# Optimization experiments

Measured on AMD Instinct MI355X. Metric: run time of the kernel, lower is better.

Reference implementation:

```python
import jax, jax.numpy as jnp
import numpy as np

N, D_IN, D_OUT, E = 8192, 1024, 1024, 8

def setup_inputs() -> dict:
    key = jax.random.key(0)
    ks = jax.random.split(key, 5)
    x = jax.random.normal(ks[0], (N, D_IN), dtype=jnp.float32)
    # expert weights stacked: [E, D_IN, D_OUT], bias [E, D_OUT]
    We = jax.random.normal(ks[1], (E, D_IN, D_OUT), dtype=jnp.float32) / np.sqrt(D_IN)
    be = jax.random.normal(ks[2], (E, D_OUT), dtype=jnp.float32) * 0.01
    # gating net: Linear(D_IN -> E)
    Wg = jax.random.normal(ks[3], (D_IN, E), dtype=jnp.float32) / np.sqrt(D_IN)
    bg = jax.random.normal(ks[4], (E,), dtype=jnp.float32) * 0.01
    return {"x": x, "We": We, "be": be, "Wg": Wg, "bg": bg}

def reference(x, We, be, Wg, bg):
    # gate: softmax over experts  [N, E]
    gate_probs = jax.nn.softmax(x @ Wg + bg, axis=-1)
    # all experts run densely on every token: [N, E, D_OUT]
    expert_out = jnp.einsum('ni,eio->neo', x, We) + be[None, :, :]
    # gate-weighted sum over experts: [N, D_OUT]
    return jnp.einsum('neo,ne->no', expert_out, gate_probs)
```

## Files before the change

kernel.cpp:

```cpp
#include <hip/hip_runtime.h>
#include <hip/hip_bf16.h>

#define N_TOK 8192
#define DIN   1024
#define DOUT  1024
#define NE    8
#define KTOT  (NE * DIN)
#define BM    128
#define BN    128
#define NKC   (KTOT / 32)

typedef __attribute__((ext_vector_type(4))) float f32x4;
typedef __attribute__((ext_vector_type(8))) short short8;
typedef unsigned int u32;

__device__ __forceinline__ ushort f2bf(float f) {
    u32 u = __float_as_uint(f);
    u32 r = (u + 0x7fffu + ((u >> 16) & 1u)) >> 16;
    return (ushort)r;
}

__device__ __forceinline__ void gload_lds16(const void* gp, void* lp) {
    __builtin_amdgcn_global_load_lds(
        (const __attribute__((address_space(1))) u32*)gp,
        (__attribute__((address_space(3))) u32*)lp, 16, 0, 0);
}

#define PH_BAR()  __builtin_amdgcn_s_barrier()
#define VMCNT4()  asm volatile("s_waitcnt vmcnt(4)" ::: "memory")
#define VMCNT0()  asm volatile("s_waitcnt vmcnt(0)" ::: "memory")

__global__ void gate_kernel(const float* __restrict__ x, const float* __restrict__ Wg,
                            const float* __restrict__ bg, float* __restrict__ g) {
    int w = threadIdx.x >> 6, lane = threadIdx.x & 63;
    int n = blockIdx.x * 4 + w;
    const float* xr = x + (size_t)n * DIN;
    float p[NE];
#pragma unroll
    for (int e = 0; e < NE; ++e) p[e] = 0.f;
    for (int i = lane; i < DIN; i += 64) {
        float xv = xr[i];
        const float* wr_ = Wg + i * NE;
#pragma unroll
        for (int e = 0; e < NE; ++e) p[e] = fmaf(xv, wr_[e], p[e]);
    }
#pragma unroll
    for (int off = 32; off > 0; off >>= 1) {
#pragma unroll
        for (int e = 0; e < NE; ++e) p[e] += __shfl_down(p[e], off);
    }
    if (lane == 0) {
        float l2[NE], m = -1e30f;
#pragma unroll
        for (int e = 0; e < NE; ++e) { l2[e] = p[e] + bg[e]; m = fmaxf(m, l2[e]); }
        float s = 0.f;
#pragma unroll
        for (int e = 0; e < NE; ++e) { l2[e] = expf(l2[e] - m); s += l2[e]; }
        float inv = 1.f / s;
#pragma unroll
        for (int e = 0; e < NE; ++e) g[n * NE + e] = l2[e] * inv;
    }
}

__global__ void transpose_w2_kernel(const float* __restrict__ We, ushort* __restrict__ B2) {
    __shared__ float tile[64][65];
    int kb = blockIdx.x * 64, ob = blockIdx.y * 64;
    int t = threadIdx.x;
#pragma unroll
    for (int ph = 0; ph < 16; ++ph) {
        int idx = ph * 256 + t;
        int r = idx >> 6, c = idx & 63;
        tile[r][c] = We[(size_t)(kb + r) * DOUT + ob + c];
    }
    __syncthreads();
#pragma unroll
    for (int ph = 0; ph < 4; ++ph) {
        int widx = ph * 256 + t;
        int o_loc = widx >> 4;
        int k_loc = (widx & 15) * 4;
        int kc = (kb + k_loc) >> 5;
        int kk = (kb + k_loc) & 31;
        ushort4 v;
        v.x = f2bf(tile[k_loc + 0][o_loc]);
        v.y = f2bf(tile[k_loc + 1][o_loc]);
        v.z = f2bf(tile[k_loc + 2][o_loc]);
        v.w = f2bf(tile[k_loc + 3][o_loc]);
        *(ushort4*)&B2[((size_t)kc * DOUT + ob + o_loc) * 32 + kk] = v;
    }
}

__global__ void prescale_kernel(const float* __restrict__ x, const float* __restrict__ g,
                                ushort* __restrict__ Ag) {
    int idx = blockIdx.x * 256 + threadIdx.x;
    int n = idx >> 7, c = idx & 127;
    float4 x0 = *(const float4*)&x[(size_t)n * DIN + c * 8];
    float4 x1 = *(const float4*)&x[(size_t)n * DIN + c * 8 + 4];
    float4 g0 = *(const float4*)&g[(size_t)n * NE + 0];
    float4 g1 = *(const float4*)&g[(size_t)n * NE + 4];
    float ge[NE] = {g0.x, g0.y, g0.z, g0.w, g1.x, g1.y, g1.z, g1.w};
#pragma unroll
    for (int e = 0; e < NE; ++e) {
        float s = ge[e];
        short8 v;
        v[0] = (short)f2bf(s * x0.x); v[1] = (short)f2bf(s * x0.y);
        v[2] = (short)f2bf(s * x0.z); v[3] = (short)f2bf(s * x0.w);
        v[4] = (short)f2bf(s * x1.x); v[5] = (short)f2bf(s * x1.y);
        v[6] = (short)f2bf(s * x1.z); v[7] = (short)f2bf(s * x1.w);
        *(short8*)&Ag[(size_t)n * KTOT + e * DIN + c * 8] = v;
    }
}

__global__ __launch_bounds__(256, 2) void moe_gemm_ps3(
    const ushort* __restrict__ Ag,
    const ushort* __restrict__ B2,
    const float*  __restrict__ g,
    const float*  __restrict__ be,
    float*        __restrict__ out)
{
    __shared__ __align__(16) ushort Al[3][BM * 32];
    __shared__ __align__(16) ushort Bl[3][BN * 32];
    __shared__ __align__(16) float  gLds[BM][NE];

    int bid = blockIdx.x;
    int swz = (bid & 7) * 64 + (bid >> 3);
    int colb = swz & 7;
    int rowb = swz >> 3;
    int brow = rowb * BM, bcol = colb * BN;

    int tid = threadIdx.x;
    int w = tid >> 6, lane = tid & 63;
    int wm = w >> 1, wn = w & 1;
    int ro = lane & 15, gq = lane >> 4;
    int jrow = gq * 4;

    ((float4*)&gLds[0][0])[tid] = ((const float4*)(g + (size_t)brow * NE))[tid];

    int offA[4], offB[4];
#pragma unroll
    for (int m = 0; m < 4; ++m) {
        int r = wm * 64 + m * 16 + ro;
        offA[m] = r * 32 + ((gq * 8) ^ ((r & 6) << 2));
    }
#pragma unroll
    for (int n = 0; n < 4; ++n) {
        int c = wn * 64 + n * 16 + ro;
        offB[n] = c * 32 + ((gq * 8) ^ ((c & 6) << 2));
    }

    auto stage = [&](int s, int K) {
#pragma unroll
        for (int L = 0; L < 2; ++L) {
            int c = L * 256 + tid;
            int row = c >> 2, slot = c & 3;
            int ks = (slot * 8) ^ ((row & 6) << 2);
            gload_lds16(Ag + (size_t)(brow + row) * KTOT + K * 32 + ks,
                        (char*)&Al[s][0] + (size_t)(c & ~63) * 16);
        }
#pragma unroll
        for (int L = 0; L < 2; ++L) {
            int c = L * 256 + tid;
            int col = c >> 2, slot = c & 3;
            int ks = (slot * 8) ^ ((col & 6) << 2);
            gload_lds16(B2 + ((size_t)K * DOUT + bcol + col) * 32 + ks,
                        (char*)&Bl[s][0] + (size_t)(c & ~63) * 16);
        }
    };

    f32x4 accP[4][4];
#pragma unroll
    for (int m = 0; m < 4; ++m)
#pragma unroll
        for (int n = 0; n < 4; ++n) accP[m][n] = (f32x4){0.f, 0.f, 0.f, 0.f};

#define PHASE(BUF, SBUF, KK, ISSUE, WAITN) do {                               \
    const ushort* _As = &Al[BUF][0];                                          \
    const ushort* _Bs = &Bl[BUF][0];                                          \
    short8 _a[4], _b[4];                                                      \
    _Pragma("unroll") for (int _m = 0; _m < 4; ++_m)                          \
        _a[_m] = *(const short8*)(_As + offA[_m]);                            \
    _Pragma("unroll") for (int _n = 0; _n < 4; ++_n)                          \
        _b[_n] = *(const short8*)(_Bs + offB[_n]);                            \
    if (ISSUE) stage(SBUF, (KK) + 2);                                         \
    __builtin_amdgcn_s_setprio(1);                                            \
    _Pragma("unroll") for (int _m = 0; _m < 4; ++_m) {                        \
        accP[_m][0] = __builtin_amdgcn_mfma_f32_16x16x32_bf16(_a[_m], _b[0], accP[_m][0], 0, 0, 0); \
        accP[_m][1] = __builtin_amdgcn_mfma_f32_16x16x32_bf16(_a[_m], _b[1], accP[_m][1], 0, 0, 0); \
        accP[_m][2] = __builtin_amdgcn_mfma_f32_16x16x32_bf16(_a[_m], _b[2], accP[_m][2], 0, 0, 0); \
        accP[_m][3] = __builtin_amdgcn_mfma_f32_16x16x32_bf16(_a[_m], _b[3], accP[_m][3], 0, 0, 0); \
    }                                                                         \
    __builtin_amdgcn_s_setprio(0);                                            \
    if ((WAITN) == 4) VMCNT4(); else if ((WAITN) == 0) VMCNT0();              \
    if ((WAITN) >= 0) PH_BAR();                                               \
} while (0)

    stage(0, 0); stage(1, 1);
    VMCNT4();
    PH_BAR();

    for (int it = 0; it < 84; ++it) {
        int k = it * 3;
        PHASE(0, 2, k + 0, 1, 4);
        PHASE(1, 0, k + 1, 1, 4);
        PHASE(2, 1, k + 2, 1, 4);
    }
    PHASE(0, 2, 252, 1, 4);
    PHASE(1, 0, 253, 1, 4);
    PHASE(2, 0, 254, 0, 0);
    PHASE(0, 0, 255, 0, -1);
#undef PHASE

#pragma unroll
    for (int m = 0; m < 4; ++m) {
#pragma unroll
        for (int j = 0; j < 4; ++j) {
            int lrow = wm * 64 + m * 16 + jrow + j;
            int grow = brow + lrow;
            float g8[NE];
#pragma unroll
            for (int e = 0; e < NE; ++e) g8[e] = gLds[lrow][e];
#pragma unroll
            for (int n = 0; n < 4; ++n) {
                int col = bcol + wn * 64 + n * 16 + ro;
                float bias = 0.f;
#pragma unroll
                for (int e = 0; e < NE; ++e) bias = fmaf(g8[e], be[e * DOUT + col], bias);
                out[(size_t)grow * DOUT + col] = accP[m][n][j] + bias;
            }
        }
    }
}

extern "C" void kernel_launch(void* const* d_in, const int* in_sizes, int n_in,
                              void* d_out, int out_size, void* d_ws, size_t ws_size,
                              hipStream_t stream) {
    const float* x  = (const float*)d_in[0];
    const float* We = (const float*)d_in[1];
    const float* be = (const float*)d_in[2];
    const float* Wg = (const float*)d_in[3];
    const float* bg = (const float*)d_in[4];
    float* out = (float*)d_out;

    char* ws = (char*)d_ws;
    const size_t GB  = 256 * 1024;
    const size_t BTB = (size_t)DOUT * KTOT * 2;
    float*  gbuf = (float*)ws;
    ushort* B2   = (ushort*)(ws + GB);
    ushort* Ag   = (ushort*)(ws + GB + BTB);

    gate_kernel<<<N_TOK / 4, 256, 0, stream>>>(x, Wg, bg, gbuf);
    transpose_w2_kernel<<<dim3(KTOT / 64, DOUT / 64), 256, 0, stream>>>(We, B2);
    prescale_kernel<<<(N_TOK * 128) / 256, 256, 0, stream>>>(x, gbuf, Ag);
    moe_gemm_ps3<<<(N_TOK / BM) * (DOUT / BN), 256, 0, stream>>>(Ag, B2, gbuf, be, out);
}
```

Measured before the change: 193.1 us.

## Enlarge GEMM tile to 256 rows and split K across two wave groups

The MoE GEMM block grows to 256x128 with 512 threads. The two wave groups each accumulate half of the K range, and one 3-stage LDS ring holds both halves' A and B tiles. Each wave now computes an 8x4 grid of MFMA tiles, which raises MFMA work per LDS fragment read and halves the number of blocks. The partial sums are reduced through LDS before the bias epilogue. In exchange this adds much larger LDS and accumulator-register use, likely limiting occupancy to one block per CU, plus an extra LDS reduction pass.

```diff
diff --git a/kernel.cpp b/kernel.cpp
--- a/kernel.cpp
+++ b/kernel.cpp
@@ -6,9 +6,10 @@
 #define DOUT  1024
 #define NE    8
 #define KTOT  (NE * DIN)
-#define BM    128
+#define BM    256
 #define BN    128
-#define NKC   (KTOT / 32)
+#define NPH   128
+#define SLOT  24576
 
 typedef __attribute__((ext_vector_type(4))) float f32x4;
 typedef __attribute__((ext_vector_type(8))) short short8;
@@ -27,7 +28,7 @@
 }
 
 #define PH_BAR()  __builtin_amdgcn_s_barrier()
-#define VMCNT4()  asm volatile("s_waitcnt vmcnt(4)" ::: "memory")
+#define VMCNT6()  asm volatile("s_waitcnt vmcnt(6)" ::: "memory")
 #define VMCNT0()  asm volatile("s_waitcnt vmcnt(0)" ::: "memory")
 
 __global__ void gate_kernel(const float* __restrict__ x, const float* __restrict__ Wg,
@@ -110,35 +111,36 @@
     }
 }
 
-__global__ __launch_bounds__(256, 2) void moe_gemm_ps3(
+__global__ __launch_bounds__(512, 2) void moe_gemm_sk(
     const ushort* __restrict__ Ag,
     const ushort* __restrict__ B2,
     const float*  __restrict__ g,
     const float*  __restrict__ be,
     float*        __restrict__ out)
 {
-    __shared__ __align__(16) ushort Al[3][BM * 32];
-    __shared__ __align__(16) ushort Bl[3][BN * 32];
+    __shared__ __align__(16) ushort ring[3][SLOT];
     __shared__ __align__(16) float  gLds[BM][NE];
 
     int bid = blockIdx.x;
-    int swz = (bid & 7) * 64 + (bid >> 3);
+    int swz = (bid & 7) * 32 + (bid >> 3);
     int colb = swz & 7;
     int rowb = swz >> 3;
     int brow = rowb * BM, bcol = colb * BN;
 
     int tid = threadIdx.x;
     int w = tid >> 6, lane = tid & 63;
-    int wm = w >> 1, wn = w & 1;
+    int wm = w >> 2, wn = (w >> 1) & 1, ks = w & 1;
     int ro = lane & 15, gq = lane >> 4;
     int jrow = gq * 4;
 
     ((float4*)&gLds[0][0])[tid] = ((const float4*)(g + (size_t)brow * NE))[tid];
 
-    int offA[4], offB[4];
-#pragma unroll
-    for (int m = 0; m < 4; ++m) {
-        int r = wm * 64 + m * 16 + ro;
+    int aoff = ks * 8192;
+    int boff = 16384 + ks * 4096;
+    int offA[8], offB[4];
+#pragma unroll
+    for (int m = 0; m < 8; ++m) {
+        int r = wm * 128 + m * 16 + ro;
         offA[m] = r * 32 + ((gq * 8) ^ ((r & 6) << 2));
     }
 #pragma unroll
@@ -147,84 +149,110 @@
         offB[n] = c * 32 + ((gq * 8) ^ ((c & 6) << 2));
     }
 
-    auto stage = [&](int s, int K) {
-#pragma unroll
-        for (int L = 0; L < 2; ++L) {
-            int c = L * 256 + tid;
-            int row = c >> 2, slot = c & 3;
-            int ks = (slot * 8) ^ ((row & 6) << 2);
-            gload_lds16(Ag + (size_t)(brow + row) * KTOT + K * 32 + ks,
-                        (char*)&Al[s][0] + (size_t)(c & ~63) * 16);
+    auto stage = [&](int s, int p) {
+        char* base = (char*)&ring[s][0];
+#pragma unroll
+        for (int ksx = 0; ksx < 2; ++ksx) {
+            int kc = ksx * NPH + p;
+#pragma unroll
+            for (int L = 0; L < 2; ++L) {
+                int q = L * 512 + tid;
+                int row = q >> 2, sl = q & 3;
+                int ksz = (sl * 8) ^ ((row & 6) << 2);
+                gload_lds16(Ag + (size_t)(brow + row) * KTOT + kc * 32 + ksz,
+                            base + ksx * 16384 + (size_t)(q & ~63) * 16);
+            }
         }
 #pragma unroll
-        for (int L = 0; L < 2; ++L) {
-            int c = L * 256 + tid;
-            int col = c >> 2, slot = c & 3;
-            int ks = (slot * 8) ^ ((col & 6) << 2);
-            gload_lds16(B2 + ((size_t)K * DOUT + bcol + col) * 32 + ks,
-                        (char*)&Bl[s][0] + (size_t)(c & ~63) * 16);
+        for (int ksx = 0; ksx < 2; ++ksx) {
+            int kc = ksx * NPH + p;
+            int q = tid;
+            int col = q >> 2, sl = q & 3;
+            int ksz = (sl * 8) ^ ((col & 6) << 2);
+            gload_lds16(B2 + ((size_t)kc * DOUT + bcol + col) * 32 + ksz,
+                        base + 32768 + ksx * 8192 + (size_t)(q & ~63) * 16);
         }
     };
 
-    f32x4 accP[4][4];
-#pragma unroll
-    for (int m = 0; m < 4; ++m)
+    f32x4 accP[8][4];
+#pragma unroll
+    for (int m = 0; m < 8; ++m)
 #pragma unroll
         for (int n = 0; n < 4; ++n) accP[m][n] = (f32x4){0.f, 0.f, 0.f, 0.f};
 
 #define PHASE(BUF, SBUF, KK, ISSUE, WAITN) do {                               \
-    const ushort* _As = &Al[BUF][0];                                          \
-    const ushort* _Bs = &Bl[BUF][0];                                          \
-    short8 _a[4], _b[4];                                                      \
-    _Pragma("unroll") for (int _m = 0; _m < 4; ++_m)                          \
+    const ushort* _As = &ring[BUF][0] + aoff;                                 \
+    const ushort* _Bs = &ring[BUF][0] + boff;                                 \
+    short8 _a[8], _b[4];                                                      \
+    _Pragma("unroll") for (int _m = 0; _m < 8; ++_m)                          \
         _a[_m] = *(const short8*)(_As + offA[_m]);                            \
     _Pragma("unroll") for (int _n = 0; _n < 4; ++_n)                          \
         _b[_n] = *(const short8*)(_Bs + offB[_n]);                            \
     if (ISSUE) stage(SBUF, (KK) + 2);                                         \
     __builtin_amdgcn_s_setprio(1);                                            \
-    _Pragma("unroll") for (int _m = 0; _m < 4; ++_m) {                        \
+    _Pragma("unroll") for (int _m = 0; _m < 8; ++_m) {                        \
         accP[_m][0] = __builtin_amdgcn_mfma_f32_16x16x32_bf16(_a[_m], _b[0], accP[_m][0], 0, 0, 0); \
         accP[_m][1] = __builtin_amdgcn_mfma_f32_16x16x32_bf16(_a[_m], _b[1], accP[_m][1], 0, 0, 0); \
         accP[_m][2] = __builtin_amdgcn_mfma_f32_16x16x32_bf16(_a[_m], _b[2], accP[_m][2], 0, 0, 0); \
         accP[_m][3] = __builtin_amdgcn_mfma_f32_16x16x32_bf16(_a[_m], _b[3], accP[_m][3], 0, 0, 0); \
     }                                                                         \
     __builtin_amdgcn_s_setprio(0);                                            \
-    if ((WAITN) == 4) VMCNT4(); else if ((WAITN) == 0) VMCNT0();              \
+    if ((WAITN) == 6) VMCNT6(); else if ((WAITN) == 0) VMCNT0();              \
     if ((WAITN) >= 0) PH_BAR();                                               \
 } while (0)
 
     stage(0, 0); stage(1, 1);
-    VMCNT4();
+    VMCNT6();
     PH_BAR();
 
-    for (int it = 0; it < 84; ++it) {
+    for (int it = 0; it < 42; ++it) {
         int k = it * 3;
-        PHASE(0, 2, k + 0, 1, 4);
-        PHASE(1, 0, k + 1, 1, 4);
-        PHASE(2, 1, k + 2, 1, 4);
-    }
-    PHASE(0, 2, 252, 1, 4);
-    PHASE(1, 0, 253, 1, 4);
-    PHASE(2, 0, 254, 0, 0);
-    PHASE(0, 0, 255, 0, -1);
+        PHASE(0, 2, k + 0, 1, 6);
+        PHASE(1, 0, k + 1, 1, 6);
+        PHASE(2, 1, k + 2, 1, 6);
+    }
+    PHASE(0, 0, 126, 0, 0);
+    PHASE(1, 0, 127, 0, -1);
 #undef PHASE
 
-#pragma unroll
-    for (int m = 0; m < 4; ++m) {
-#pragma unroll
-        for (int j = 0; j < 4; ++j) {
-            int lrow = wm * 64 + m * 16 + jrow + j;
-            int grow = brow + lrow;
-            float g8[NE];
-#pragma unroll
-            for (int e = 0; e < NE; ++e) g8[e] = gLds[lrow][e];
-#pragma unroll
-            for (int n = 0; n < 4; ++n) {
-                int col = bcol + wn * 64 + n * 16 + ro;
-                float bias = 0.f;
-#pragma unroll
-                for (int e = 0; e < NE; ++e) bias = fmaf(g8[e], be[e * DOUT + col], bias);
-                out[(size_t)grow * DOUT + col] = accP[m][n][j] + bias;
+    __syncthreads();
+    int pairIdx = wm * 2 + wn;
+    float* red = (float*)&ring[0][0];
+    if (ks == 1) {
+#pragma unroll
+        for (int m = 0; m < 8; ++m)
+#pragma unroll
+            for (int j = 0; j < 4; ++j) {
+                int lr = m * 16 + jrow + j;
+#pragma unroll
+                for (int n = 0; n < 4; ++n) {
+                    int lc = n * 16 + ro;
+                    red[pairIdx * 8192 + lr * 64 + lc] = accP[m][n][j];
+                }
+            }
+    }
+    __syncthreads();
+    if (ks == 0) {
+#pragma unroll
+        for (int m = 0; m < 8; ++m) {
+#pragma unroll
+            for (int j = 0; j < 4; ++j) {
+                int lr = m * 16 + jrow + j;
+                int lrow = wm * 128 + lr;
+                int grow = brow + lrow;
+                float g8[NE];
+#pragma unroll
+                for (int e = 0; e < NE; ++e) g8[e] = gLds[lrow][e];
+#pragma unroll
+                for (int n = 0; n < 4; ++n) {
+                    int lc = n * 16 + ro;
+                    int col = bcol + wn * 64 + lc;
+                    float bias = 0.f;
+#pragma unroll
+                    for (int e = 0; e < NE; ++e) bias = fmaf(g8[e], be[e * DOUT + col], bias);
+                    out[(size_t)grow * DOUT + col] =
+                        accP[m][n][j] + red[pairIdx * 8192 + lr * 64 + lc] + bias;
+                }
             }
         }
     }
@@ -250,5 +278,5 @@
     gate_kernel<<<N_TOK / 4, 256, 0, stream>>>(x, Wg, bg, gbuf);
     transpose_w2_kernel<<<dim3(KTOT / 64, DOUT / 64), 256, 0, stream>>>(We, B2);
     prescale_kernel<<<(N_TOK * 128) / 256, 256, 0, stream>>>(x, gbuf, Ag);
-    moe_gemm_ps3<<<(N_TOK / BM) * (DOUT / BN), 256, 0, stream>>>(Ag, B2, gbuf, be, out);
-}
+    moe_gemm_sk<<<(N_TOK / BM) * (DOUT / BN), 512, 0, stream>>>(Ag, B2, gbuf, be, out);
+}
```

New measurement: 192.9 us. Within noise of the previous version (-0.1%).
